# Performance work log

Hardware: AMD Instinct MI355X
Metric: run time of the kernel (lower is better)

The kernel has to match this reference:

```python
import jax, jax.numpy as jnp
import numpy as np

HIDDEN = 1024
FFN = 3584
NUM_EXPERTS = 8
TOP_K = 2
B, S = 2, 1024


def setup_inputs() -> dict:
    key = jax.random.key(0)
    k0, k1, k2, k3 = jax.random.split(key, 4)
    hidden_states = jax.random.normal(k0, (B, S, HIDDEN), dtype=jnp.float32)
    # torch Linear stores [out, in]; we keep gate as [E, H] (matches nn.Linear weight)
    gate_w = jax.random.normal(k1, (NUM_EXPERTS, HIDDEN), dtype=jnp.float32) * 0.02
    # GroupedLinear weights stored as [E, in, out] for direct x @ W per expert
    w_gate_up = jax.random.normal(k2, (NUM_EXPERTS, HIDDEN, 2 * FFN), dtype=jnp.float32) * 0.02
    w_down = jax.random.normal(k3, (NUM_EXPERTS, FFN, HIDDEN), dtype=jnp.float32) * 0.02
    return {"hidden_states": hidden_states, "gate_w": gate_w,
            "w_gate_up": w_gate_up, "w_down": w_down}


def reference(hidden_states, gate_w, w_gate_up, w_down):
    b, s, h = hidden_states.shape
    x = hidden_states.reshape(-1, h)                      # [T, H]
    T = x.shape[0]
    E = gate_w.shape[0]

    # Router: logits -> fp32 softmax -> top-k -> renormalize (Mixtral semantics)
    router_logits = x @ gate_w.T                          # [T, E]
    probs = jax.nn.softmax(router_logits.astype(jnp.float32), axis=-1)
    top_vals, top_idx = jax.lax.top_k(probs, TOP_K)       # [T, K]
    top_vals = top_vals / top_vals.sum(axis=-1, keepdims=True)
    top_vals = top_vals.astype(x.dtype)

    # Dense combine weights [T, E]: scatter top-k probs to expert slots.
    # Equivalent to permute -> grouped GEMM -> unpermute-with-probs.
    combine = jnp.zeros((T, E), dtype=x.dtype).at[
        jnp.arange(T)[:, None], top_idx].add(top_vals)

    out = jnp.zeros_like(x)
    for e in range(E):  # fixed small expert count
        gu = x @ w_gate_up[e]                             # [T, 2F]
        gate_proj, up_proj = jnp.split(gu, 2, axis=-1)
        act = jax.nn.silu(gate_proj) * up_proj            # [T, F]
        out = out + combine[:, e:e + 1] * (act @ w_down[e])

    return out.reshape(b, s, h), router_logits
```

## Files before the change

kernel.cpp:

```cpp
#include <hip/hip_runtime.h>
#include <hip/hip_bf16.h>
#include <stdint.h>

#define HIDDEN  1024
#define FFN     3584
#define NE      8
#define NTOK    2048
#define CAP     2048
#define OUT_ELEMS (NTOK * HIDDEN)

#define X_OFF   0u
#define CNT_OFF (4u*1024u*1024u)
#define TOK_OFF (CNT_OFF + 256u)
#define WGT_OFF (TOK_OFF + 65536u)
#define ACT_OFF (WGT_OFF + 65536u)

typedef __attribute__((ext_vector_type(8))) short short8;
typedef __attribute__((ext_vector_type(4))) float floatx4;

static __device__ __forceinline__ uint32_t f2bf(float f) {
  union { float f; uint32_t u; } v; v.f = f;
  return (v.u + 0x7FFFu + ((v.u >> 16) & 1u)) >> 16;
}
static __device__ __forceinline__ uint32_t pack2(float lo, float hi) {
  return f2bf(lo) | (f2bf(hi) << 16);
}
union S8U { uint4 u; short8 s; };
static __device__ __forceinline__ short8 as_short8(uint4 v) { S8U x; x.u = v; return x.s; }

__global__ __launch_bounds__(256) void moe_prep(float4* __restrict__ out4,
                                                int* __restrict__ cnt) {
  uint32_t i = blockIdx.x * 256u + threadIdx.x;
  out4[i] = make_float4(0.f, 0.f, 0.f, 0.f);
  if (blockIdx.x == 0 && threadIdx.x < NE) cnt[threadIdx.x] = 0;
}

__global__ __launch_bounds__(256) void moe_convert(const float4* __restrict__ x4,
                                                   uint4* __restrict__ xb) {
  uint32_t g = blockIdx.x * 256u + threadIdx.x;
  float4 a = x4[2u*g], b = x4[2u*g + 1u];
  xb[g] = make_uint4(pack2(a.x, a.y), pack2(a.z, a.w),
                     pack2(b.x, b.y), pack2(b.z, b.w));
}

__global__ __launch_bounds__(256) void moe_router(
    const float* __restrict__ x, const float* __restrict__ gw,
    float* __restrict__ logits, int* __restrict__ cnt,
    int* __restrict__ tok, float* __restrict__ wgt)
{
  const int t = blockIdx.x * 4 + (threadIdx.x >> 6);
  const int lane = threadIdx.x & 63;
  const float* xr = x + (size_t)t * HIDDEN;
  float a[NE];
#pragma unroll
  for (int e = 0; e < NE; ++e) a[e] = 0.f;
  for (int hh = 0; hh < HIDDEN / 64; ++hh) {
    float xv = xr[hh * 64 + lane];
#pragma unroll
    for (int e = 0; e < NE; ++e) a[e] += xv * gw[e * HIDDEN + hh * 64 + lane];
  }
#pragma unroll
  for (int off = 32; off > 0; off >>= 1) {
#pragma unroll
    for (int e = 0; e < NE; ++e) a[e] += __shfl_xor(a[e], off);
  }
  if (lane == 0) {
#pragma unroll
    for (int e = 0; e < NE; ++e) logits[t * NE + e] = a[e];
    int i0 = 0; float v0 = a[0];
#pragma unroll
    for (int e = 1; e < NE; ++e) if (a[e] > v0) { v0 = a[e]; i0 = e; }
    int i1 = (i0 == 0) ? 1 : 0; float v1 = a[i1];
#pragma unroll
    for (int e = 0; e < NE; ++e) if (e != i0 && a[e] > v1) { v1 = a[e]; i1 = e; }
    float w0 = 1.f / (1.f + __expf(v1 - v0));
    float w1 = 1.f - w0;
    int p0 = atomicAdd(&cnt[i0], 1); tok[i0 * CAP + p0] = t; wgt[i0 * CAP + p0] = w0;
    int p1 = atomicAdd(&cnt[i1], 1); tok[i1 * CAP + p1] = t; wgt[i1 * CAP + p1] = w1;
  }
}

__global__ __launch_bounds__(256) void moe_gateup(
    const uint4* __restrict__ xb, const float* __restrict__ wgu,
    const int* __restrict__ cnt, const int* __restrict__ tok,
    unsigned short* __restrict__ act)
{
  const int e  = blockIdx.z;
  const int m0 = blockIdx.y * 128;
  const int f0 = blockIdx.x * 64;
  const int cn = cnt[e];
  if (m0 >= cn) return;
  int basev = 0;
#pragma unroll
  for (int i = 0; i < NE; ++i) { int ci = cnt[i]; if (i < e) basev += ci; }

  __shared__ uint4    As[1024];
  __shared__ uint32_t Bs[4096];

  const int tid  = threadIdx.x;
  const int lane = tid & 63;
  const int w    = tid >> 6;
  const int wm   = w >> 1, wn = w & 1;
  const int q    = lane >> 4;
  const int c    = lane & 15;

  floatx4 acc[4][4];
#pragma unroll
  for (int i = 0; i < 4; ++i)
#pragma unroll
    for (int j = 0; j < 4; ++j) acc[i][j] = (floatx4){0.f, 0.f, 0.f, 0.f};

  const float* wB  = wgu + (size_t)e * HIDDEN * (2 * FFN);
  const int* tokE  = tok + e * CAP;

  for (int kt = 0; kt < HIDDEN / 64; ++kt) {
    const int k0 = kt * 64;
    __syncthreads();
#pragma unroll
    for (int it = 0; it < 4; ++it) {
      int cid = it * 256 + tid;
      int row = cid >> 3, c8 = cid & 7;
      int mrow = m0 + row; if (mrow >= cn) mrow = cn - 1;
      int tk = tokE[mrow];
      As[row * 8 + (c8 ^ (row & 7))] = xb[(size_t)tk * (HIDDEN / 8) + (k0 >> 3) + c8];
    }
#pragma unroll
    for (int it = 0; it < 4; ++it) {
      int mid = it * 256 + tid;
      int kp = mid >> 5;
      int n  = (mid & 31) * 4;
      int col = f0 + ((n >> 6) << 5) + (n & 31) + (((n >> 5) & 1) ? FFN : 0);
      const float* src = wB + (size_t)(k0 + 2 * kp) * (2 * FFN) + col;
      float4 r0 = *(const float4*)src;
      float4 r1 = *(const float4*)(src + 2 * FFN);
      int widx = kp * 128 + (n ^ (((kp >> 2) & 1) << 4));
      *(uint4*)&Bs[widx] = make_uint4(pack2(r0.x, r1.x), pack2(r0.y, r1.y),
                                      pack2(r0.z, r1.z), pack2(r0.w, r1.w));
    }
    __syncthreads();
#pragma unroll
    for (int ks = 0; ks < 2; ++ks) {
      short8 af[4];
#pragma unroll
      for (int i = 0; i < 4; ++i) {
        int row = wm * 64 + i * 16 + c;
        int kc8 = ks * 4 + q;
        af[i] = as_short8(As[row * 8 + (kc8 ^ (row & 7))]);
      }
      short8 bfr[4];
#pragma unroll
      for (int j = 0; j < 4; ++j) {
        int n  = wn * 64 + j * 16 + c;
        int kp = ks * 16 + q * 4;
        int nn = n ^ ((q & 1) << 4);
        bfr[j] = as_short8(make_uint4(Bs[(kp + 0) * 128 + nn], Bs[(kp + 1) * 128 + nn],
                                      Bs[(kp + 2) * 128 + nn], Bs[(kp + 3) * 128 + nn]));
      }
#pragma unroll
      for (int i = 0; i < 4; ++i)
#pragma unroll
        for (int j = 0; j < 4; ++j)
          acc[i][j] = __builtin_amdgcn_mfma_f32_16x16x32_bf16(af[i], bfr[j], acc[i][j], 0, 0, 0);
    }
  }

#pragma unroll
  for (int i = 0; i < 4; ++i) {
#pragma unroll
    for (int r = 0; r < 4; ++r) {
      int m = m0 + wm * 64 + i * 16 + q * 4 + r;
      if (m < cn) {
#pragma unroll
        for (int j = 0; j < 2; ++j) {
          float g = acc[i][j][r];
          float u = acc[i][j + 2][r];
          float a = (g / (1.f + __expf(-g))) * u;
          act[(size_t)(basev + m) * FFN + (f0 + wn * 32 + j * 16 + c)] = (unsigned short)f2bf(a);
        }
      }
    }
  }
}

__global__ __launch_bounds__(256) void moe_down(
    const uint4* __restrict__ actc, const float* __restrict__ wd,
    const int* __restrict__ cnt, const int* __restrict__ tok,
    const float* __restrict__ wgt, float* __restrict__ out)
{
  const int e  = blockIdx.z;
  const int m0 = blockIdx.y * 128;
  const int n0 = blockIdx.x * 128;
  const int cn = cnt[e];
  if (m0 >= cn) return;
  int basev = 0;
#pragma unroll
  for (int i = 0; i < NE; ++i) { int ci = cnt[i]; if (i < e) basev += ci; }

  __shared__ uint4    As[1024];
  __shared__ uint32_t Bs[4096];

  const int tid  = threadIdx.x;
  const int lane = tid & 63;
  const int w    = tid >> 6;
  const int wm   = w >> 1, wn = w & 1;
  const int q    = lane >> 4;
  const int c    = lane & 15;

  floatx4 acc[4][4];
#pragma unroll
  for (int i = 0; i < 4; ++i)
#pragma unroll
    for (int j = 0; j < 4; ++j) acc[i][j] = (floatx4){0.f, 0.f, 0.f, 0.f};

  const float* wB = wd + (size_t)e * FFN * HIDDEN;

  for (int kt = 0; kt < FFN / 64; ++kt) {
    const int k0 = kt * 64;
    __syncthreads();
#pragma unroll
    for (int it = 0; it < 4; ++it) {
      int cid = it * 256 + tid;
      int row = cid >> 3, c8 = cid & 7;
      int mrow = m0 + row; if (mrow >= cn) mrow = cn - 1;
      As[row * 8 + (c8 ^ (row & 7))] =
          actc[(size_t)(basev + mrow) * (FFN / 8) + (k0 >> 3) + c8];
    }
#pragma unroll
    for (int it = 0; it < 4; ++it) {
      int mid = it * 256 + tid;
      int kp = mid >> 5;
      int n  = (mid & 31) * 4;
      int col = n0 + n;
      const float* src = wB + (size_t)(k0 + 2 * kp) * HIDDEN + col;
      float4 r0 = *(const float4*)src;
      float4 r1 = *(const float4*)(src + HIDDEN);
      int widx = kp * 128 + (n ^ (((kp >> 2) & 1) << 4));
      *(uint4*)&Bs[widx] = make_uint4(pack2(r0.x, r1.x), pack2(r0.y, r1.y),
                                      pack2(r0.z, r1.z), pack2(r0.w, r1.w));
    }
    __syncthreads();
#pragma unroll
    for (int ks = 0; ks < 2; ++ks) {
      short8 af[4];
#pragma unroll
      for (int i = 0; i < 4; ++i) {
        int row = wm * 64 + i * 16 + c;
        int kc8 = ks * 4 + q;
        af[i] = as_short8(As[row * 8 + (kc8 ^ (row & 7))]);
      }
      short8 bfr[4];
#pragma unroll
      for (int j = 0; j < 4; ++j) {
        int n  = wn * 64 + j * 16 + c;
        int kp = ks * 16 + q * 4;
        int nn = n ^ ((q & 1) << 4);
        bfr[j] = as_short8(make_uint4(Bs[(kp + 0) * 128 + nn], Bs[(kp + 1) * 128 + nn],
                                      Bs[(kp + 2) * 128 + nn], Bs[(kp + 3) * 128 + nn]));
      }
#pragma unroll
      for (int i = 0; i < 4; ++i)
#pragma unroll
        for (int j = 0; j < 4; ++j)
          acc[i][j] = __builtin_amdgcn_mfma_f32_16x16x32_bf16(af[i], bfr[j], acc[i][j], 0, 0, 0);
    }
  }

#pragma unroll
  for (int i = 0; i < 4; ++i) {
#pragma unroll
    for (int r = 0; r < 4; ++r) {
      int m = m0 + wm * 64 + i * 16 + q * 4 + r;
      if (m < cn) {
        int   t  = tok[e * CAP + m];
        float wg = wgt[e * CAP + m];
        float* orow = out + (size_t)t * HIDDEN + n0 + wn * 64 + c;
#pragma unroll
        for (int j = 0; j < 4; ++j)
          atomicAdd(orow + j * 16, acc[i][j][r] * wg);
      }
    }
  }
}

extern "C" void kernel_launch(void* const* d_in, const int* in_sizes, int n_in,
                              void* d_out, int out_size, void* d_ws, size_t ws_size,
                              hipStream_t stream)
{
  (void)in_sizes; (void)n_in; (void)out_size; (void)ws_size;
  const float* x   = (const float*)d_in[0];
  const float* gw  = (const float*)d_in[1];
  const float* wgu = (const float*)d_in[2];
  const float* wd  = (const float*)d_in[3];
  float* out = (float*)d_out;
  char*  ws  = (char*)d_ws;

  uint4*          xb  = (uint4*)(ws + X_OFF);
  int*            cnt = (int*)(ws + CNT_OFF);
  int*            tok = (int*)(ws + TOK_OFF);
  float*          wgt = (float*)(ws + WGT_OFF);
  unsigned short* act = (unsigned short*)(ws + ACT_OFF);

  moe_prep<<<OUT_ELEMS / (256 * 4), 256, 0, stream>>>((float4*)out, cnt);
  moe_convert<<<(NTOK * HIDDEN) / (256 * 8), 256, 0, stream>>>((const float4*)x, xb);
  moe_router<<<NTOK / 4, 256, 0, stream>>>(x, gw, out + OUT_ELEMS, cnt, tok, wgt);
  moe_gateup<<<dim3(FFN / 64, 16, NE), 256, 0, stream>>>(xb, wgu, cnt, tok, act);
  moe_down<<<dim3(HIDDEN / 128, 16, NE), 256, 0, stream>>>((const uint4*)act, wd, cnt, tok, wgt, out);
}
```

Measured before the change: 631.8 us.

## Pre-convert expert weights to swizzled bf16 tiles and load via global_load_lds

Adds two kernels that convert the fp32 expert weights into bf16 tiles, pre-packed in k-pairs and pre-swizzled, in workspace on every call. The GEMM kernels then stream A and B tiles straight into LDS with global_load_lds. This removes the per-block fp32 load-and-convert work and the register staging of the weights, and it halves the bytes read inside the GEMM loop. The cost is an extra full pass over all fp32 weights (about 235MB read, 117MB written) on every call. It also needs a larger workspace, and the old path remains as a fallback when the workspace is too small.

```diff
diff --git a/kernel.cpp b/kernel.cpp
--- a/kernel.cpp
+++ b/kernel.cpp
@@ -14,6 +14,12 @@
 #define TOK_OFF (CNT_OFF + 256u)
 #define WGT_OFF (TOK_OFF + 65536u)
 #define ACT_OFF (WGT_OFF + 65536u)
+#define ACT_SZ  (4096u * 3584u * 2u)
+#define WGU_OFF (ACT_OFF + ACT_SZ)
+#define WGU_SZ  (8u*56u*16u*16384u)
+#define WDB_OFF (WGU_OFF + WGU_SZ)
+#define WDB_SZ  (8u*8u*56u*16384u)
+#define WS_NEED ((size_t)WDB_OFF + (size_t)WDB_SZ)
 
 typedef __attribute__((ext_vector_type(8))) short short8;
 typedef __attribute__((ext_vector_type(4))) float floatx4;
@@ -27,6 +33,12 @@
 }
 union S8U { uint4 u; short8 s; };
 static __device__ __forceinline__ short8 as_short8(uint4 v) { S8U x; x.u = v; return x.s; }
+
+static __device__ __forceinline__ void ld_g2l16(const void* g, void* l) {
+  __builtin_amdgcn_global_load_lds(
+      (const __attribute__((address_space(1))) void*)g,
+      (__attribute__((address_space(3))) void*)l, 16, 0, 0);
+}
 
 __global__ __launch_bounds__(256) void moe_prep(float4* __restrict__ out4,
                                                 int* __restrict__ cnt) {
@@ -80,7 +92,241 @@
   }
 }
 
+__global__ __launch_bounds__(256) void moe_wconv_gu(const float* __restrict__ wgu,
+                                                    uint4* __restrict__ wgub) {
+  const int kt = blockIdx.x, fb = blockIdx.y, e = blockIdx.z;
+  const int f0 = fb * 64, k0 = kt * 64;
+  const float* wB = wgu + (size_t)e * HIDDEN * (2 * FFN);
+  uint4* dst = wgub + ((size_t)(e * 56 + fb) * 16 + kt) * 1024;
+#pragma unroll
+  for (int it = 0; it < 4; ++it) {
+    int mid = it * 256 + threadIdx.x;
+    int kp = mid >> 5;
+    int n  = (mid & 31) * 4;
+    int col = f0 + ((n >> 6) << 5) + (n & 31) + (((n >> 5) & 1) ? FFN : 0);
+    const float* src = wB + (size_t)(k0 + 2 * kp) * (2 * FFN) + col;
+    float4 r0 = *(const float4*)src;
+    float4 r1 = *(const float4*)(src + 2 * FFN);
+    dst[kp * 32 + ((n >> 2) ^ (((kp >> 2) & 1) << 2))] =
+        make_uint4(pack2(r0.x, r1.x), pack2(r0.y, r1.y),
+                   pack2(r0.z, r1.z), pack2(r0.w, r1.w));
+  }
+}
+
+__global__ __launch_bounds__(256) void moe_wconv_d(const float* __restrict__ wd,
+                                                   uint4* __restrict__ wdb) {
+  const int kt = blockIdx.x, nb = blockIdx.y, e = blockIdx.z;
+  const int n0 = nb * 128, k0 = kt * 64;
+  const float* wB = wd + (size_t)e * FFN * HIDDEN;
+  uint4* dst = wdb + ((size_t)(e * 8 + nb) * 56 + kt) * 1024;
+#pragma unroll
+  for (int it = 0; it < 4; ++it) {
+    int mid = it * 256 + threadIdx.x;
+    int kp = mid >> 5;
+    int n  = (mid & 31) * 4;
+    const float* src = wB + (size_t)(k0 + 2 * kp) * HIDDEN + n0 + n;
+    float4 r0 = *(const float4*)src;
+    float4 r1 = *(const float4*)(src + HIDDEN);
+    dst[kp * 32 + ((n >> 2) ^ (((kp >> 2) & 1) << 2))] =
+        make_uint4(pack2(r0.x, r1.x), pack2(r0.y, r1.y),
+                   pack2(r0.z, r1.z), pack2(r0.w, r1.w));
+  }
+}
+
 __global__ __launch_bounds__(256) void moe_gateup(
+    const uint4* __restrict__ xb, const uint4* __restrict__ wgub,
+    const int* __restrict__ cnt, const int* __restrict__ tok,
+    unsigned short* __restrict__ act)
+{
+  const int e  = blockIdx.z;
+  const int m0 = blockIdx.y * 128;
+  const int fb = blockIdx.x;
+  const int f0 = fb * 64;
+  const int cn = cnt[e];
+  if (m0 >= cn) return;
+  int basev = 0;
+#pragma unroll
+  for (int i = 0; i < NE; ++i) { int ci = cnt[i]; if (i < e) basev += ci; }
+
+  __shared__ uint4 As[1024];
+  __shared__ uint4 Bs4[1024];
+  const uint32_t* Bs = (const uint32_t*)Bs4;
+
+  const int tid  = threadIdx.x;
+  const int lane = tid & 63;
+  const int w    = tid >> 6;
+  const int wm   = w >> 1, wn = w & 1;
+  const int q    = lane >> 4;
+  const int c    = lane & 15;
+
+  const int* tokE = tok + e * CAP;
+  const char* aptr[4];
+#pragma unroll
+  for (int it = 0; it < 4; ++it) {
+    int p   = (w * 4 + it) * 64 + lane;
+    int row = p >> 3, c8 = p & 7;
+    int mrow = m0 + row; if (mrow >= cn) mrow = cn - 1;
+    aptr[it] = (const char*)(xb + (size_t)tokE[mrow] * (HIDDEN / 8) + (c8 ^ (row & 7)));
+  }
+  const char* bptr = (const char*)wgub + ((size_t)(e * 56 + fb) * 16) * 16384u
+                   + (size_t)w * 4096u + (size_t)lane * 16u;
+
+  floatx4 acc[4][4];
+#pragma unroll
+  for (int i = 0; i < 4; ++i)
+#pragma unroll
+    for (int j = 0; j < 4; ++j) acc[i][j] = (floatx4){0.f, 0.f, 0.f, 0.f};
+
+  for (int kt = 0; kt < HIDDEN / 64; ++kt) {
+    __syncthreads();
+#pragma unroll
+    for (int it = 0; it < 4; ++it)
+      ld_g2l16(aptr[it] + (size_t)kt * 128u, &As[(w * 4 + it) * 64]);
+#pragma unroll
+    for (int it = 0; it < 4; ++it)
+      ld_g2l16(bptr + (size_t)kt * 16384u + (size_t)it * 1024u, &Bs4[(w * 4 + it) * 64]);
+    __syncthreads();
+#pragma unroll
+    for (int ks = 0; ks < 2; ++ks) {
+      short8 af[4];
+#pragma unroll
+      for (int i = 0; i < 4; ++i) {
+        int row = wm * 64 + i * 16 + c;
+        int kc8 = ks * 4 + q;
+        af[i] = as_short8(As[row * 8 + (kc8 ^ (row & 7))]);
+      }
+      short8 bfr[4];
+#pragma unroll
+      for (int j = 0; j < 4; ++j) {
+        int n  = wn * 64 + j * 16 + c;
+        int kp = ks * 16 + q * 4;
+        int nn = n ^ ((q & 1) << 4);
+        bfr[j] = as_short8(make_uint4(Bs[(kp + 0) * 128 + nn], Bs[(kp + 1) * 128 + nn],
+                                      Bs[(kp + 2) * 128 + nn], Bs[(kp + 3) * 128 + nn]));
+      }
+#pragma unroll
+      for (int i = 0; i < 4; ++i)
+#pragma unroll
+        for (int j = 0; j < 4; ++j)
+          acc[i][j] = __builtin_amdgcn_mfma_f32_16x16x32_bf16(af[i], bfr[j], acc[i][j], 0, 0, 0);
+    }
+  }
+
+#pragma unroll
+  for (int i = 0; i < 4; ++i) {
+#pragma unroll
+    for (int r = 0; r < 4; ++r) {
+      int m = m0 + wm * 64 + i * 16 + q * 4 + r;
+      if (m < cn) {
+#pragma unroll
+        for (int j = 0; j < 2; ++j) {
+          float g = acc[i][j][r];
+          float u = acc[i][j + 2][r];
+          float a = (g / (1.f + __expf(-g))) * u;
+          act[(size_t)(basev + m) * FFN + (f0 + wn * 32 + j * 16 + c)] = (unsigned short)f2bf(a);
+        }
+      }
+    }
+  }
+}
+
+__global__ __launch_bounds__(256) void moe_down(
+    const unsigned short* __restrict__ act, const uint4* __restrict__ wdb,
+    const int* __restrict__ cnt, const int* __restrict__ tok,
+    const float* __restrict__ wgt, float* __restrict__ out)
+{
+  const int e  = blockIdx.z;
+  const int m0 = blockIdx.y * 128;
+  const int nb = blockIdx.x;
+  const int n0 = nb * 128;
+  const int cn = cnt[e];
+  if (m0 >= cn) return;
+  int basev = 0;
+#pragma unroll
+  for (int i = 0; i < NE; ++i) { int ci = cnt[i]; if (i < e) basev += ci; }
+
+  __shared__ uint4 As[1024];
+  __shared__ uint4 Bs4[1024];
+  const uint32_t* Bs = (const uint32_t*)Bs4;
+
+  const int tid  = threadIdx.x;
+  const int lane = tid & 63;
+  const int w    = tid >> 6;
+  const int wm   = w >> 1, wn = w & 1;
+  const int q    = lane >> 4;
+  const int c    = lane & 15;
+
+  const char* aptr[4];
+#pragma unroll
+  for (int it = 0; it < 4; ++it) {
+    int p   = (w * 4 + it) * 64 + lane;
+    int row = p >> 3, c8 = p & 7;
+    int mrow = m0 + row; if (mrow >= cn) mrow = cn - 1;
+    aptr[it] = (const char*)act +
+               ((size_t)(basev + mrow) * FFN + (size_t)((c8 ^ (row & 7)) * 8)) * 2u;
+  }
+  const char* bptr = (const char*)wdb + ((size_t)(e * 8 + nb) * 56) * 16384u
+                   + (size_t)w * 4096u + (size_t)lane * 16u;
+
+  floatx4 acc[4][4];
+#pragma unroll
+  for (int i = 0; i < 4; ++i)
+#pragma unroll
+    for (int j = 0; j < 4; ++j) acc[i][j] = (floatx4){0.f, 0.f, 0.f, 0.f};
+
+  for (int kt = 0; kt < FFN / 64; ++kt) {
+    __syncthreads();
+#pragma unroll
+    for (int it = 0; it < 4; ++it)
+      ld_g2l16(aptr[it] + (size_t)kt * 128u, &As[(w * 4 + it) * 64]);
+#pragma unroll
+    for (int it = 0; it < 4; ++it)
+      ld_g2l16(bptr + (size_t)kt * 16384u + (size_t)it * 1024u, &Bs4[(w * 4 + it) * 64]);
+    __syncthreads();
+#pragma unroll
+    for (int ks = 0; ks < 2; ++ks) {
+      short8 af[4];
+#pragma unroll
+      for (int i = 0; i < 4; ++i) {
+        int row = wm * 64 + i * 16 + c;
+        int kc8 = ks * 4 + q;
+        af[i] = as_short8(As[row * 8 + (kc8 ^ (row & 7))]);
+      }
+      short8 bfr[4];
+#pragma unroll
+      for (int j = 0; j < 4; ++j) {
+        int n  = wn * 64 + j * 16 + c;
+        int kp = ks * 16 + q * 4;
+        int nn = n ^ ((q & 1) << 4);
+        bfr[j] = as_short8(make_uint4(Bs[(kp + 0) * 128 + nn], Bs[(kp + 1) * 128 + nn],
+                                      Bs[(kp + 2) * 128 + nn], Bs[(kp + 3) * 128 + nn]));
+      }
+#pragma unroll
+      for (int i = 0; i < 4; ++i)
+#pragma unroll
+        for (int j = 0; j < 4; ++j)
+          acc[i][j] = __builtin_amdgcn_mfma_f32_16x16x32_bf16(af[i], bfr[j], acc[i][j], 0, 0, 0);
+    }
+  }
+
+#pragma unroll
+  for (int i = 0; i < 4; ++i) {
+#pragma unroll
+    for (int r = 0; r < 4; ++r) {
+      int m = m0 + wm * 64 + i * 16 + q * 4 + r;
+      if (m < cn) {
+        int   t  = tok[e * CAP + m];
+        float wg = wgt[e * CAP + m];
+        float* orow = out + (size_t)t * HIDDEN + n0 + wn * 64 + c;
+#pragma unroll
+        for (int j = 0; j < 4; ++j)
+          atomicAdd(orow + j * 16, acc[i][j][r] * wg);
+      }
+    }
+  }
+}
+
+__global__ __launch_bounds__(256) void moe_gateup_lg(
     const uint4* __restrict__ xb, const float* __restrict__ wgu,
     const int* __restrict__ cnt, const int* __restrict__ tok,
     unsigned short* __restrict__ act)
@@ -182,7 +428,7 @@
   }
 }
 
-__global__ __launch_bounds__(256) void moe_down(
+__global__ __launch_bounds__(256) void moe_down_lg(
     const uint4* __restrict__ actc, const float* __restrict__ wd,
     const int* __restrict__ cnt, const int* __restrict__ tok,
     const float* __restrict__ wgt, float* __restrict__ out)
@@ -286,7 +532,7 @@
                               void* d_out, int out_size, void* d_ws, size_t ws_size,
                               hipStream_t stream)
 {
-  (void)in_sizes; (void)n_in; (void)out_size; (void)ws_size;
+  (void)in_sizes; (void)n_in; (void)out_size;
   const float* x   = (const float*)d_in[0];
   const float* gw  = (const float*)d_in[1];
   const float* wgu = (const float*)d_in[2];
@@ -294,15 +540,27 @@
   float* out = (float*)d_out;
   char*  ws  = (char*)d_ws;
 
-  uint4*          xb  = (uint4*)(ws + X_OFF);
-  int*            cnt = (int*)(ws + CNT_OFF);
-  int*            tok = (int*)(ws + TOK_OFF);
-  float*          wgt = (float*)(ws + WGT_OFF);
-  unsigned short* act = (unsigned short*)(ws + ACT_OFF);
+  uint4*          xb   = (uint4*)(ws + X_OFF);
+  int*            cnt  = (int*)(ws + CNT_OFF);
+  int*            tok  = (int*)(ws + TOK_OFF);
+  float*          wgt  = (float*)(ws + WGT_OFF);
+  unsigned short* act  = (unsigned short*)(ws + ACT_OFF);
+  uint4*          wgub = (uint4*)(ws + WGU_OFF);
+  uint4*          wdb  = (uint4*)(ws + WDB_OFF);
+
+  const bool fast = (ws_size >= WS_NEED);
 
   moe_prep<<<OUT_ELEMS / (256 * 4), 256, 0, stream>>>((float4*)out, cnt);
   moe_convert<<<(NTOK * HIDDEN) / (256 * 8), 256, 0, stream>>>((const float4*)x, xb);
   moe_router<<<NTOK / 4, 256, 0, stream>>>(x, gw, out + OUT_ELEMS, cnt, tok, wgt);
-  moe_gateup<<<dim3(FFN / 64, 16, NE), 256, 0, stream>>>(xb, wgu, cnt, tok, act);
-  moe_down<<<dim3(HIDDEN / 128, 16, NE), 256, 0, stream>>>((const uint4*)act, wd, cnt, tok, wgt, out);
-}
+
+  if (fast) {
+    moe_wconv_gu<<<dim3(16, 56, NE), 256, 0, stream>>>(wgu, wgub);
+    moe_wconv_d<<<dim3(56, 8, NE), 256, 0, stream>>>(wd, wdb);
+    moe_gateup<<<dim3(FFN / 64, 16, NE), 256, 0, stream>>>(xb, wgub, cnt, tok, act);
+    moe_down<<<dim3(HIDDEN / 128, 16, NE), 256, 0, stream>>>(act, wdb, cnt, tok, wgt, out);
+  } else {
+    moe_gateup_lg<<<dim3(FFN / 64, 16, NE), 256, 0, stream>>>(xb, wgu, cnt, tok, act);
+    moe_down_lg<<<dim3(HIDDEN / 128, 16, NE), 256, 0, stream>>>((const uint4*)act, wd, cnt, tok, wgt, out);
+  }
+}
```

New measurement: 670.0 us. 1.06x slower.
